# Performance work log

Measured on AMD Instinct MI355X. Metric: run time of the kernel, lower is better.

## Reference

```python
import jax, jax.numpy as jnp
import numpy as np

SCALE_WEIGHT = 0.5 ** 0.5
B, C, T, S = 8, 512, 2048, 2048


def setup_inputs() -> dict:
    key = jax.random.key(0)
    ks = jax.random.split(key, 6)
    return {
        "base_target_emb": jax.random.normal(ks[0], (B, C, T, 1), dtype=jnp.float32),
        "input_from_dec": jax.random.normal(ks[1], (B, C, T, 1), dtype=jnp.float32),
        "encoder_out_top": jax.random.normal(ks[2], (B, C, S), dtype=jnp.float32),
        "encoder_out_combine": jax.random.normal(ks[3], (B, C, S), dtype=jnp.float32),
        "W": jax.random.normal(ks[4], (C, C), dtype=jnp.float32) * (1.0 / np.sqrt(C)),
        "b": jax.random.normal(ks[5], (C,), dtype=jnp.float32) * 0.01,
    }


def reference(base_target_emb, input_from_dec, encoder_out_top, encoder_out_combine, W, b):
    # seq_linear: per-token Linear over the channel dim. torch Linear: h = x @ W.T + b, W is [out,in]
    x = input_from_dec[..., 0]                                # [B,C,T]
    preatt = jnp.einsum('oc,bct->bot', W, x) + b[None, :, None]  # [B,C,T]
    target = (base_target_emb[..., 0] + preatt) * SCALE_WEIGHT   # [B,C,T]
    pre_attn = jnp.einsum('bct,bcs->bts', target, encoder_out_top)  # [B,T,S]
    attn = jax.nn.softmax(pre_attn, axis=2)                      # [B,T,S]
    ctx = jnp.einsum('bts,bcs->btc', attn, encoder_out_combine)  # [B,T,C]
    context_output = jnp.transpose(ctx, (0, 2, 1))[..., None]    # [B,C,T,1]
    return context_output, attn
```

## Files before the change

kernel.cpp:

```cpp
#include <hip/hip_runtime.h>
#include <cstddef>
#include <cstdint>

#define SCALE_WEIGHT 0.70710678118654752440f

static constexpr int B_ = 8, C_ = 512, T_ = 2048, S_ = 2048;
static constexpr size_t BCT_ = (size_t)B_ * C_ * T_;
static constexpr size_t BTS_ = (size_t)B_ * T_ * S_;

typedef _Float16 half_t;
typedef half_t half8  __attribute__((ext_vector_type(8)));
typedef half_t half4v __attribute__((ext_vector_type(4)));
typedef float  floatx4 __attribute__((ext_vector_type(4)));

__device__ __forceinline__ void gload_lds16(const void* g, void* l) {
    __builtin_amdgcn_global_load_lds(
        (const __attribute__((address_space(1))) void*)g,
        (__attribute__((address_space(3))) void*)l, 16, 0, 0);
}

__global__ __launch_bounds__(256) void transpose_cvt_kernel(
    const float* __restrict__ in, half_t* __restrict__ out, int R, int Cc)
{
    __shared__ float tile[32][33];
    const int b  = blockIdx.z;
    const int r0 = blockIdx.y * 32, c0 = blockIdx.x * 32;
    const float* ib = in + (size_t)b * R * Cc;
    half_t* ob = out + (size_t)b * R * Cc;
    const int tx = threadIdx.x & 31, ty = threadIdx.x >> 5;
    #pragma unroll
    for (int i = 0; i < 4; ++i)
        tile[ty + i * 8][tx] = ib[(size_t)(r0 + ty + i * 8) * Cc + c0 + tx];
    __syncthreads();
    #pragma unroll
    for (int i = 0; i < 4; ++i)
        ob[(size_t)(c0 + ty + i * 8) * R + r0 + tx] = (half_t)tile[tx][ty + i * 8];
}

__global__ __launch_bounds__(256) void cvt_f32_f16_kernel(
    const float* __restrict__ in, half_t* __restrict__ out, int n4)
{
    const int stride = gridDim.x * blockDim.x;
    for (int i = blockIdx.x * blockDim.x + threadIdx.x; i < n4; i += stride) {
        float4 v = ((const float4*)in)[i];
        half4v h = {(half_t)v.x, (half_t)v.y, (half_t)v.z, (half_t)v.w};
        ((half4v*)out)[i] = h;
    }
}

template<int EPI>
__global__ __launch_bounds__(256) void gemm_f16_kernel(
    const half_t* __restrict__ A, const half_t* __restrict__ Bm,
    float* __restrict__ Cout, half_t* __restrict__ CoutH,
    const float* __restrict__ base, const float* __restrict__ bias,
    int M, int N, int K, size_t sA, size_t sB, size_t sC)
{
    __shared__ __align__(128) half_t As[128 * 32];
    __shared__ __align__(128) half_t Bs[128 * 32];

    const int tid  = threadIdx.x;
    const int lane = tid & 63, w = tid >> 6;
    const int wr = w >> 1, wc = w & 1;
    const int b  = blockIdx.z;
    const int m0 = blockIdx.y * 128, n0 = blockIdx.x * 128;

    const half_t* Ab = A  + (size_t)b * sA;
    const half_t* Bb = Bm + (size_t)b * sB;

    const int w2  = w * 2;
    const int mR0 = w2 * 16 + (lane >> 2);
    const int mR1 = mR0 + 16;
    const int kgd = lane & 3;
    const int kgs0 = kgd ^ ((mR0 >> 1) & 3);
    const int kgs1 = kgd ^ ((mR1 >> 1) & 3);
    const half_t* aSrc0 = Ab + (size_t)(m0 + mR0) * K + kgs0 * 8;
    const half_t* aSrc1 = Ab + (size_t)(m0 + mR1) * K + kgs1 * 8;
    const half_t* bSrc0 = Bb + (size_t)(n0 + mR0) * K + kgs0 * 8;
    const half_t* bSrc1 = Bb + (size_t)(n0 + mR1) * K + kgs1 * 8;
    char* AsB = (char*)As;
    char* BsB = (char*)Bs;
    char* dA0 = AsB + (w2 + 0) * 1024;
    char* dA1 = AsB + (w2 + 1) * 1024;
    char* dB0 = BsB + (w2 + 0) * 1024;
    char* dB1 = BsB + (w2 + 1) * 1024;

    const int fr = lane & 15, kg = lane >> 4;
    int aoff[4], boff[4];
    #pragma unroll
    for (int mi = 0; mi < 4; ++mi) {
        int m = wr * 64 + mi * 16 + fr;
        aoff[mi] = m * 64 + ((kg ^ ((m >> 1) & 3)) << 4);
    }
    #pragma unroll
    for (int nj = 0; nj < 4; ++nj) {
        int n = wc * 64 + nj * 16 + fr;
        boff[nj] = n * 64 + ((kg ^ ((n >> 1) & 3)) << 4);
    }

    floatx4 acc[4][4];
    #pragma unroll
    for (int mi = 0; mi < 4; ++mi)
        #pragma unroll
        for (int nj = 0; nj < 4; ++nj)
            acc[mi][nj] = (floatx4){0.f, 0.f, 0.f, 0.f};

    for (int k0 = 0; k0 < K; k0 += 32) {
        __syncthreads();
        gload_lds16(aSrc0 + k0, dA0);
        gload_lds16(aSrc1 + k0, dA1);
        gload_lds16(bSrc0 + k0, dB0);
        gload_lds16(bSrc1 + k0, dB1);
        __syncthreads();

        half8 af[4], bf[4];
        #pragma unroll
        for (int mi = 0; mi < 4; ++mi) af[mi] = *(const half8*)(AsB + aoff[mi]);
        #pragma unroll
        for (int nj = 0; nj < 4; ++nj) bf[nj] = *(const half8*)(BsB + boff[nj]);
        #pragma unroll
        for (int mi = 0; mi < 4; ++mi)
            #pragma unroll
            for (int nj = 0; nj < 4; ++nj)
                acc[mi][nj] = __builtin_amdgcn_mfma_f32_16x16x32_f16(
                    af[mi], bf[nj], acc[mi][nj], 0, 0, 0);
    }

    if constexpr (EPI == 0) {
        float* Cb = Cout + (size_t)b * sC;
        #pragma unroll
        for (int mi = 0; mi < 4; ++mi) {
            const int row = m0 + wr * 64 + mi * 16 + (lane >> 4) * 4;
            #pragma unroll
            for (int nj = 0; nj < 4; ++nj) {
                const int col = n0 + wc * 64 + nj * 16 + (lane & 15);
                #pragma unroll
                for (int r = 0; r < 4; ++r)
                    Cb[(size_t)(row + r) * N + col] = acc[mi][nj][r];
            }
        }
    } else {
        half_t* Cb = CoutH + (size_t)b * sC;
        #pragma unroll
        for (int nj = 0; nj < 4; ++nj) {
            const int col = n0 + wc * 64 + nj * 16 + (lane & 15);
            const float bn = bias[col];
            const float* bp = base + ((size_t)b * N + col) * (size_t)M;
            #pragma unroll
            for (int mi = 0; mi < 4; ++mi) {
                const int row = m0 + wr * 64 + mi * 16 + (lane >> 4) * 4;
                #pragma unroll
                for (int r = 0; r < 4; ++r) {
                    float v = (acc[mi][nj][r] + bn + bp[row + r]) * SCALE_WEIGHT;
                    Cb[(size_t)(row + r) * N + col] = (half_t)v;
                }
            }
        }
    }
}

__global__ __launch_bounds__(256) void k3_softmax_kernel(
    float* __restrict__ logits, half_t* __restrict__ attnh)
{
    float* p = logits + (size_t)blockIdx.x * S_;
    half4v* ph = (half4v*)(attnh + (size_t)blockIdx.x * S_);
    const int tid = threadIdx.x;
    float4 v0 = *(const float4*)&p[tid * 4];
    float4 v1 = *(const float4*)&p[tid * 4 + 1024];

    float mx = fmaxf(fmaxf(fmaxf(v0.x, v0.y), fmaxf(v0.z, v0.w)),
                     fmaxf(fmaxf(v1.x, v1.y), fmaxf(v1.z, v1.w)));
    #pragma unroll
    for (int off = 32; off; off >>= 1)
        mx = fmaxf(mx, __shfl_xor(mx, off));

    __shared__ float sm[4];
    __shared__ float ss[4];
    const int wid = tid >> 6, lane = tid & 63;
    if (lane == 0) sm[wid] = mx;
    __syncthreads();
    const float rmax = fmaxf(fmaxf(sm[0], sm[1]), fmaxf(sm[2], sm[3]));

    float e[8];
    e[0] = expf(v0.x - rmax); e[1] = expf(v0.y - rmax);
    e[2] = expf(v0.z - rmax); e[3] = expf(v0.w - rmax);
    e[4] = expf(v1.x - rmax); e[5] = expf(v1.y - rmax);
    e[6] = expf(v1.z - rmax); e[7] = expf(v1.w - rmax);

    float sum = 0.f;
    #pragma unroll
    for (int i = 0; i < 8; ++i) sum += e[i];
    #pragma unroll
    for (int off = 32; off; off >>= 1)
        sum += __shfl_xor(sum, off);
    if (lane == 0) ss[wid] = sum;
    __syncthreads();
    const float inv = 1.f / (ss[0] + ss[1] + ss[2] + ss[3]);

    float4 r0, r1;
    r0.x = e[0] * inv; r0.y = e[1] * inv; r0.z = e[2] * inv; r0.w = e[3] * inv;
    r1.x = e[4] * inv; r1.y = e[5] * inv; r1.z = e[6] * inv; r1.w = e[7] * inv;
    *(float4*)&p[tid * 4] = r0;
    *(float4*)&p[tid * 4 + 1024] = r1;
    ph[tid]       = (half4v){(half_t)r0.x, (half_t)r0.y, (half_t)r0.z, (half_t)r0.w};
    ph[tid + 256] = (half4v){(half_t)r1.x, (half_t)r1.y, (half_t)r1.z, (half_t)r1.w};
}

extern "C" void kernel_launch(void* const* d_in, const int* in_sizes, int n_in,
                              void* d_out, int out_size, void* d_ws, size_t ws_size,
                              hipStream_t stream) {
    const float* base = (const float*)d_in[0];
    const float* x    = (const float*)d_in[1];
    const float* top  = (const float*)d_in[2];
    const float* comb = (const float*)d_in[3];
    const float* W    = (const float*)d_in[4];
    const float* bias = (const float*)d_in[5];

    float* out    = (float*)d_out;
    float* ctx    = out;
    float* logits = out + BCT_;

    half_t* xT   = (half_t*)d_out;
    half_t* topT = xT + BCT_;

    half_t* attnh = (half_t*)d_ws;
    half_t* tgtT  = attnh;
    half_t* combh = attnh + BTS_;
    half_t* Wh    = combh + (size_t)B_ * C_ * S_;

    transpose_cvt_kernel<<<dim3(T_ / 32, C_ / 32, B_), 256, 0, stream>>>(x, xT, C_, T_);
    transpose_cvt_kernel<<<dim3(S_ / 32, C_ / 32, B_), 256, 0, stream>>>(top, topT, C_, S_);
    cvt_f32_f16_kernel<<<2048, 256, 0, stream>>>(comb, combh, (int)((size_t)B_ * C_ * S_ / 4));
    cvt_f32_f16_kernel<<<256, 256, 0, stream>>>(W, Wh, C_ * C_ / 4);

    gemm_f16_kernel<1><<<dim3(C_ / 128, T_ / 128, B_), 256, 0, stream>>>(
        xT, Wh, nullptr, tgtT, base, bias,
        T_, C_, C_, (size_t)T_ * C_, 0, (size_t)T_ * C_);

    gemm_f16_kernel<0><<<dim3(S_ / 128, T_ / 128, B_), 256, 0, stream>>>(
        tgtT, topT, logits, nullptr, nullptr, nullptr,
        T_, S_, C_, (size_t)T_ * C_, (size_t)S_ * C_, (size_t)T_ * S_);

    k3_softmax_kernel<<<dim3(B_ * T_), 256, 0, stream>>>(logits, attnh);

    gemm_f16_kernel<0><<<dim3(T_ / 128, C_ / 128, B_), 256, 0, stream>>>(
        combh, attnh, ctx, nullptr, nullptr, nullptr,
        C_, T_, S_, (size_t)C_ * S_, (size_t)T_ * S_, (size_t)C_ * T_);
}
```

Baseline: 246.7 us.

## Double-buffer GEMM LDS tiles with K=64 stages, vectorize transpose, use fast exp

New measurement: 212.0 us. 1.16x faster.

```diff
diff --git a/kernel.cpp b/kernel.cpp
--- a/kernel.cpp
+++ b/kernel.cpp
@@ -22,19 +22,31 @@
 __global__ __launch_bounds__(256) void transpose_cvt_kernel(
     const float* __restrict__ in, half_t* __restrict__ out, int R, int Cc)
 {
-    __shared__ float tile[32][33];
+    __shared__ float tile[64][65];
     const int b  = blockIdx.z;
-    const int r0 = blockIdx.y * 32, c0 = blockIdx.x * 32;
+    const int r0 = blockIdx.y * 64, c0 = blockIdx.x * 64;
     const float* ib = in + (size_t)b * R * Cc;
     half_t* ob = out + (size_t)b * R * Cc;
-    const int tx = threadIdx.x & 31, ty = threadIdx.x >> 5;
-    #pragma unroll
-    for (int i = 0; i < 4; ++i)
-        tile[ty + i * 8][tx] = ib[(size_t)(r0 + ty + i * 8) * Cc + c0 + tx];
+    const int t  = threadIdx.x;
+    const int rr = t >> 4, cq = t & 15;
+    #pragma unroll
+    for (int i = 0; i < 4; ++i) {
+        const int r = rr + i * 16;
+        float4 v = *(const float4*)&ib[(size_t)(r0 + r) * Cc + c0 + cq * 4];
+        tile[cq * 4 + 0][r] = v.x;
+        tile[cq * 4 + 1][r] = v.y;
+        tile[cq * 4 + 2][r] = v.z;
+        tile[cq * 4 + 3][r] = v.w;
+    }
     __syncthreads();
-    #pragma unroll
-    for (int i = 0; i < 4; ++i)
-        ob[(size_t)(c0 + ty + i * 8) * R + r0 + tx] = (half_t)tile[tx][ty + i * 8];
+    const int cw = t >> 4, rq = (t & 15) * 4;
+    #pragma unroll
+    for (int i = 0; i < 4; ++i) {
+        const int c = cw + i * 16;
+        half4v h = {(half_t)tile[c][rq + 0], (half_t)tile[c][rq + 1],
+                    (half_t)tile[c][rq + 2], (half_t)tile[c][rq + 3]};
+        *(half4v*)&ob[(size_t)(c0 + c) * R + r0 + rq] = h;
+    }
 }
 
 __global__ __launch_bounds__(256) void cvt_f32_f16_kernel(
@@ -49,14 +61,14 @@
 }
 
 template<int EPI>
-__global__ __launch_bounds__(256) void gemm_f16_kernel(
+__global__ __launch_bounds__(256) void gemm_f16_db_kernel(
     const half_t* __restrict__ A, const half_t* __restrict__ Bm,
     float* __restrict__ Cout, half_t* __restrict__ CoutH,
     const float* __restrict__ base, const float* __restrict__ bias,
     int M, int N, int K, size_t sA, size_t sB, size_t sC)
 {
-    __shared__ __align__(128) half_t As[128 * 32];
-    __shared__ __align__(128) half_t Bs[128 * 32];
+    __shared__ __align__(128) half_t As[2][128 * 64];
+    __shared__ __align__(128) half_t Bs[2][128 * 64];
 
     const int tid  = threadIdx.x;
     const int lane = tid & 63, w = tid >> 6;
@@ -67,34 +79,29 @@
     const half_t* Ab = A  + (size_t)b * sA;
     const half_t* Bb = Bm + (size_t)b * sB;
 
-    const int w2  = w * 2;
-    const int mR0 = w2 * 16 + (lane >> 2);
-    const int mR1 = mR0 + 16;
-    const int kgd = lane & 3;
-    const int kgs0 = kgd ^ ((mR0 >> 1) & 3);
-    const int kgs1 = kgd ^ ((mR1 >> 1) & 3);
-    const half_t* aSrc0 = Ab + (size_t)(m0 + mR0) * K + kgs0 * 8;
-    const half_t* aSrc1 = Ab + (size_t)(m0 + mR1) * K + kgs1 * 8;
-    const half_t* bSrc0 = Bb + (size_t)(n0 + mR0) * K + kgs0 * 8;
-    const half_t* bSrc1 = Bb + (size_t)(n0 + mR1) * K + kgs1 * 8;
-    char* AsB = (char*)As;
-    char* BsB = (char*)Bs;
-    char* dA0 = AsB + (w2 + 0) * 1024;
-    char* dA1 = AsB + (w2 + 1) * 1024;
-    char* dB0 = BsB + (w2 + 0) * 1024;
-    char* dB1 = BsB + (w2 + 1) * 1024;
+    const int lr = lane >> 3;
+    const int sw = (lane & 7) ^ lr;
+    const half_t* aG[4]; const half_t* bG[4];
+    int dOff[4];
+    #pragma unroll
+    for (int i = 0; i < 4; ++i) {
+        const int r = w * 32 + i * 8 + lr;
+        aG[i] = Ab + (size_t)(m0 + r) * K + sw * 8;
+        bG[i] = Bb + (size_t)(n0 + r) * K + sw * 8;
+        dOff[i] = (w * 32 + i * 8) * 128;
+    }
 
     const int fr = lane & 15, kg = lane >> 4;
     int aoff[4], boff[4];
     #pragma unroll
     for (int mi = 0; mi < 4; ++mi) {
-        int m = wr * 64 + mi * 16 + fr;
-        aoff[mi] = m * 64 + ((kg ^ ((m >> 1) & 3)) << 4);
+        const int m = wr * 64 + mi * 16 + fr;
+        aoff[mi] = m * 128 + ((kg ^ (m & 7)) << 4);
     }
     #pragma unroll
     for (int nj = 0; nj < 4; ++nj) {
-        int n = wc * 64 + nj * 16 + fr;
-        boff[nj] = n * 64 + ((kg ^ ((n >> 1) & 3)) << 4);
+        const int n = wc * 64 + nj * 16 + fr;
+        boff[nj] = n * 128 + ((kg ^ (n & 7)) << 4);
     }
 
     floatx4 acc[4][4];
@@ -104,26 +111,57 @@
         for (int nj = 0; nj < 4; ++nj)
             acc[mi][nj] = (floatx4){0.f, 0.f, 0.f, 0.f};
 
-    for (int k0 = 0; k0 < K; k0 += 32) {
-        __syncthreads();
-        gload_lds16(aSrc0 + k0, dA0);
-        gload_lds16(aSrc1 + k0, dA1);
-        gload_lds16(bSrc0 + k0, dB0);
-        gload_lds16(bSrc1 + k0, dB1);
-        __syncthreads();
-
-        half8 af[4], bf[4];
-        #pragma unroll
-        for (int mi = 0; mi < 4; ++mi) af[mi] = *(const half8*)(AsB + aoff[mi]);
-        #pragma unroll
-        for (int nj = 0; nj < 4; ++nj) bf[nj] = *(const half8*)(BsB + boff[nj]);
-        #pragma unroll
-        for (int mi = 0; mi < 4; ++mi)
+    auto STAGE = [&](int t, int pg) {
+        const int k0 = t * 64;
+        char* Ad = (char*)As[pg];
+        char* Bd = (char*)Bs[pg];
+        #pragma unroll
+        for (int i = 0; i < 4; ++i) {
+            gload_lds16(aG[i] + k0, Ad + dOff[i]);
+            gload_lds16(bG[i] + k0, Bd + dOff[i]);
+        }
+    };
+
+    auto COMPUTE = [&](int pg) {
+        const char* Ar = (const char*)As[pg];
+        const char* Br = (const char*)Bs[pg];
+        #pragma unroll
+        for (int kk = 0; kk < 2; ++kk) {
+            half8 af[4], bf[4];
+            #pragma unroll
+            for (int mi = 0; mi < 4; ++mi)
+                af[mi] = *(const half8*)(Ar + (aoff[mi] ^ (kk << 6)));
             #pragma unroll
             for (int nj = 0; nj < 4; ++nj)
-                acc[mi][nj] = __builtin_amdgcn_mfma_f32_16x16x32_f16(
-                    af[mi], bf[nj], acc[mi][nj], 0, 0, 0);
-    }
+                bf[nj] = *(const half8*)(Br + (boff[nj] ^ (kk << 6)));
+            #pragma unroll
+            for (int mi = 0; mi < 4; ++mi)
+                #pragma unroll
+                for (int nj = 0; nj < 4; ++nj)
+                    acc[mi][nj] = __builtin_amdgcn_mfma_f32_16x16x32_f16(
+                        af[mi], bf[nj], acc[mi][nj], 0, 0, 0);
+        }
+    };
+
+    const int NT = K >> 6;
+    STAGE(0, 0);
+    int cur = 0;
+    for (int t = 0; t < NT - 1; ++t) {
+        STAGE(t + 1, cur ^ 1);
+        asm volatile("s_waitcnt vmcnt(8)" ::: "memory");
+        __builtin_amdgcn_s_barrier();
+        __builtin_amdgcn_sched_barrier(0);
+        COMPUTE(cur);
+        asm volatile("s_waitcnt lgkmcnt(0)" ::: "memory");
+        __builtin_amdgcn_sched_barrier(0);
+        __builtin_amdgcn_s_barrier();
+        __builtin_amdgcn_sched_barrier(0);
+        cur ^= 1;
+    }
+    asm volatile("s_waitcnt vmcnt(0)" ::: "memory");
+    __builtin_amdgcn_s_barrier();
+    __builtin_amdgcn_sched_barrier(0);
+    COMPUTE(cur);
 
     if constexpr (EPI == 0) {
         float* Cb = Cout + (size_t)b * sC;
@@ -181,10 +219,10 @@
     const float rmax = fmaxf(fmaxf(sm[0], sm[1]), fmaxf(sm[2], sm[3]));
 
     float e[8];
-    e[0] = expf(v0.x - rmax); e[1] = expf(v0.y - rmax);
-    e[2] = expf(v0.z - rmax); e[3] = expf(v0.w - rmax);
-    e[4] = expf(v1.x - rmax); e[5] = expf(v1.y - rmax);
-    e[6] = expf(v1.z - rmax); e[7] = expf(v1.w - rmax);
+    e[0] = __expf(v0.x - rmax); e[1] = __expf(v0.y - rmax);
+    e[2] = __expf(v0.z - rmax); e[3] = __expf(v0.w - rmax);
+    e[4] = __expf(v1.x - rmax); e[5] = __expf(v1.y - rmax);
+    e[6] = __expf(v1.z - rmax); e[7] = __expf(v1.w - rmax);
 
     float sum = 0.f;
     #pragma unroll
@@ -227,22 +265,22 @@
     half_t* combh = attnh + BTS_;
     half_t* Wh    = combh + (size_t)B_ * C_ * S_;
 
-    transpose_cvt_kernel<<<dim3(T_ / 32, C_ / 32, B_), 256, 0, stream>>>(x, xT, C_, T_);
-    transpose_cvt_kernel<<<dim3(S_ / 32, C_ / 32, B_), 256, 0, stream>>>(top, topT, C_, S_);
+    transpose_cvt_kernel<<<dim3(T_ / 64, C_ / 64, B_), 256, 0, stream>>>(x, xT, C_, T_);
+    transpose_cvt_kernel<<<dim3(S_ / 64, C_ / 64, B_), 256, 0, stream>>>(top, topT, C_, S_);
     cvt_f32_f16_kernel<<<2048, 256, 0, stream>>>(comb, combh, (int)((size_t)B_ * C_ * S_ / 4));
     cvt_f32_f16_kernel<<<256, 256, 0, stream>>>(W, Wh, C_ * C_ / 4);
 
-    gemm_f16_kernel<1><<<dim3(C_ / 128, T_ / 128, B_), 256, 0, stream>>>(
+    gemm_f16_db_kernel<1><<<dim3(C_ / 128, T_ / 128, B_), 256, 0, stream>>>(
         xT, Wh, nullptr, tgtT, base, bias,
         T_, C_, C_, (size_t)T_ * C_, 0, (size_t)T_ * C_);
 
-    gemm_f16_kernel<0><<<dim3(S_ / 128, T_ / 128, B_), 256, 0, stream>>>(
+    gemm_f16_db_kernel<0><<<dim3(S_ / 128, T_ / 128, B_), 256, 0, stream>>>(
         tgtT, topT, logits, nullptr, nullptr, nullptr,
         T_, S_, C_, (size_t)T_ * C_, (size_t)S_ * C_, (size_t)T_ * S_);
 
     k3_softmax_kernel<<<dim3(B_ * T_), 256, 0, stream>>>(logits, attnh);
 
-    gemm_f16_kernel<0><<<dim3(T_ / 128, C_ / 128, B_), 256, 0, stream>>>(
+    gemm_f16_db_kernel<0><<<dim3(T_ / 128, C_ / 128, B_), 256, 0, stream>>>(
         combh, attnh, ctx, nullptr, nullptr, nullptr,
         C_, T_, S_, (size_t)C_ * S_, (size_t)T_ * S_, (size_t)C_ * T_);
 }
```
